# Kernel optimization log

Measured on AMD Instinct MI355X. Metric: run time of the kernel, lower is better.

The kernel has to match this reference:

```python
import jax, jax.numpy as jnp
import numpy as np

D_MODEL = 1024
N_HEAD = 16
ATT_DIM = D_MODEL // N_HEAD  # 64
B, S = 8, 2048


def setup_inputs() -> dict:
    key = jax.random.key(0)
    kq, kk, kv, kwq, kwk, kwv = jax.random.split(key, 6)
    # xavier_uniform bound for Linear(hidden_dim -> att_dim)
    bound = float(np.sqrt(6.0 / (D_MODEL + ATT_DIM)))
    return {
        "q": jax.random.normal(kq, (B, S, D_MODEL), dtype=jnp.float32),
        "k": jax.random.normal(kk, (B, S, D_MODEL), dtype=jnp.float32),
        "v": jax.random.normal(kv, (B, S, D_MODEL), dtype=jnp.float32),
        "Wq": jax.random.uniform(kwq, (ATT_DIM, D_MODEL), jnp.float32, -bound, bound),
        "Wk": jax.random.uniform(kwk, (ATT_DIM, D_MODEL), jnp.float32, -bound, bound),
        "Wv": jax.random.uniform(kwv, (ATT_DIM, D_MODEL), jnp.float32, -bound, bound),
    }


def reference(q, k, v, Wq, Wk, Wv):
    # Linear projections (no bias): [B,S,d_model] @ [d_model,att_dim]
    qp = jnp.einsum('bsd,ed->bse', q, Wq)
    kp = jnp.einsum('bsd,ed->bse', k, Wk)
    vp = jnp.einsum('bsd,ed->bse', v, Wv)
    # Scores: note original divides by att_dim (not sqrt)
    scores = jnp.einsum('bqe,bke->bqk', qp, kp) / ATT_DIM
    probs = jax.nn.softmax(scores, axis=-1)  # [B,S,S]
    att = jnp.einsum('bqk,bke->bqe', probs, vp)  # [B,S,att_dim]
    # dropout is identity in eval mode
    return (att, probs)
```

## Files before the change

### kernel.cpp

```cpp
#include <hip/hip_runtime.h>
#include <hip/hip_bf16.h>

#define D_MODEL 1024
#define ATT_DIM 64
#define BATCH 8
#define SEQ 2048
#define MROWS (BATCH * SEQ)

typedef short bf16x8 __attribute__((ext_vector_type(8)));
typedef float f32x4 __attribute__((ext_vector_type(4)));

#define MFMA16(a, b, c) __builtin_amdgcn_mfma_f32_16x16x32_bf16((a), (b), (c), 0, 0, 0)

__device__ inline short f2bf(float f) {
    union { __hip_bfloat16 h; short s; } u;
    u.h = __float2bfloat16(f);
    return u.s;
}

__device__ __forceinline__ unsigned cvtpk(float lo, float hi) {
    unsigned r;
    asm("v_cvt_pk_bf16_f32 %0, %1, %2" : "=v"(r) : "v"(lo), "v"(hi));
    return r;
}

__device__ __forceinline__ void gload_lds16(const void* g, void* l) {
    __builtin_amdgcn_global_load_lds(
        (const __attribute__((address_space(1))) void*)g,
        (__attribute__((address_space(3))) void*)l, 16, 0, 0);
}

__global__ __launch_bounds__(256) void wcvt_kernel(
    const float* __restrict__ Wq, const float* __restrict__ Wk,
    const float* __restrict__ Wv, short* __restrict__ Wbf)
{
    const int idx = blockIdx.x * 256 + threadIdx.x;
    const int per = ATT_DIM * D_MODEL;
    const int base = idx * 8;
    const int mi = base / per;
    const int off = base - mi * per;
    const float* src = (mi == 0) ? Wq : (mi == 1 ? Wk : Wv);
    const float sc = (mi == 0) ? (1.0f / 64.0f) : 1.0f;
    const float4 a = *reinterpret_cast<const float4*>(src + off);
    const float4 b = *reinterpret_cast<const float4*>(src + off + 4);
    bf16x8 r;
    r[0] = f2bf(a.x * sc); r[1] = f2bf(a.y * sc);
    r[2] = f2bf(a.z * sc); r[3] = f2bf(a.w * sc);
    r[4] = f2bf(b.x * sc); r[5] = f2bf(b.y * sc);
    r[6] = f2bf(b.z * sc); r[7] = f2bf(b.w * sc);
    *reinterpret_cast<bf16x8*>(Wbf + base) = r;
}

__global__ __launch_bounds__(256) void proj_mfma_kernel(
    const float* __restrict__ q, const float* __restrict__ k,
    const float* __restrict__ v, const short* __restrict__ Wbf,
    short* __restrict__ qp, short* __restrict__ kp, short* __restrict__ vpT)
{
    const int mat = blockIdx.y;
    const float* x = (mat == 0) ? q : (mat == 1 ? k : v);
    const short* W = Wbf + mat * ATT_DIM * D_MODEL;

    __shared__ float As[2][4096];

    const int tid = threadIdx.x;
    const int w = tid >> 6;
    const int l = tid & 63;
    const int lr = l & 15;
    const int g = l >> 4;

    const int m0 = blockIdx.x * 64;
    const int row = w * 16 + lr;
    const int xr = (row & 7) << 4;

    f32x4 acc[4] = {};

    #define STAGE(c, buf)                                                      \
        {                                                                      \
            const int kt_ = (c) * 64;                                          \
            _Pragma("unroll")                                                  \
            for (int j = 0; j < 4; ++j) {                                      \
                const int rs = (w * 4 + j) * 4 + g;                            \
                const int scb = (lr * 16) ^ ((rs & 7) << 4);                   \
                gload_lds16(x + (long)(m0 + rs) * D_MODEL + kt_ + (scb >> 2),  \
                            &As[buf][(w * 4 + j) * 256]);                      \
            }                                                                  \
        }

    STAGE(0, 0);
    __syncthreads();

    for (int c = 0; c < 16; ++c) {
        const int buf = c & 1;
        if (c < 15) STAGE(c + 1, buf ^ 1);

        const int kt = c * 64;
        const char* Ab = (const char*)&As[buf][0] + row * 256;
        #pragma unroll
        for (int ks = 0; ks < 2; ++ks) {
            const int b0 = ks * 128 + g * 32;
            const float4 a0 = *reinterpret_cast<const float4*>(Ab + (b0 ^ xr));
            const float4 a1 = *reinterpret_cast<const float4*>(Ab + ((b0 + 16) ^ xr));
            bf16x8 af;
            af[0] = f2bf(a0.x); af[1] = f2bf(a0.y); af[2] = f2bf(a0.z); af[3] = f2bf(a0.w);
            af[4] = f2bf(a1.x); af[5] = f2bf(a1.y); af[6] = f2bf(a1.z); af[7] = f2bf(a1.w);
            #pragma unroll
            for (int ef = 0; ef < 4; ++ef) {
                const bf16x8 wf = *reinterpret_cast<const bf16x8*>(
                    W + (ef * 16 + lr) * D_MODEL + kt + ks * 32 + g * 8);
                acc[ef] = MFMA16(af, wf, acc[ef]);
            }
        }
        __syncthreads();
    }
    #undef STAGE

    if (mat < 2) {
        short* out = (mat == 0) ? qp : kp;
        #pragma unroll
        for (int ef = 0; ef < 4; ++ef)
            #pragma unroll
            for (int j = 0; j < 4; ++j)
                out[(long)(m0 + w * 16 + g * 4 + j) * ATT_DIM + ef * 16 + lr] =
                    f2bf(acc[ef][j]);
    } else {
        const int b = m0 / SEQ;
        const int s0 = (m0 - b * SEQ) + w * 16;
        #pragma unroll
        for (int ef = 0; ef < 4; ++ef)
            #pragma unroll
            for (int j = 0; j < 4; ++j)
                vpT[((long)b * ATT_DIM + ef * 16 + lr) * SEQ + s0 + g * 4 + j] =
                    f2bf(acc[ef][j]);
    }
}

__global__ __launch_bounds__(512, 4) void attn_kernel(
    const short* __restrict__ qp, const short* __restrict__ kp,
    const short* __restrict__ vpT, float* __restrict__ probs,
    float* __restrict__ att)
{
    __shared__ float stats_l[8][16];
    __shared__ float lds_o[8][64][17];

    const int tid = threadIdx.x;
    const int w = tid >> 6;
    const int l = tid & 63;
    const int lr = l & 15;
    const int g = l >> 4;

    const int b = blockIdx.y;
    const int q0 = blockIdx.x * 16;

    const short* qpb = qp + ((long)b * SEQ + q0) * ATT_DIM;
    const short* kpb = kp + (long)b * SEQ * ATT_DIM;
    const short* vTb = vpT + (long)b * ATT_DIM * SEQ;

    const bf16x8 qa0 = *reinterpret_cast<const bf16x8*>(qpb + lr * ATT_DIM + g * 8);
    const bf16x8 qa1 = *reinterpret_cast<const bf16x8*>(qpb + lr * ATT_DIM + 32 + g * 8);

    const int kbeg = w * 256;

    f32x4 s[8][2];
    #pragma unroll
    for (int ch = 0; ch < 8; ++ch) {
        const short* kb = kpb + (long)(kbeg + ch * 32) * ATT_DIM;
        const bf16x8 kb00 = *reinterpret_cast<const bf16x8*>(kb + lr * ATT_DIM + g * 8);
        const bf16x8 kb01 = *reinterpret_cast<const bf16x8*>(kb + lr * ATT_DIM + 32 + g * 8);
        const bf16x8 kb10 = *reinterpret_cast<const bf16x8*>(kb + (16 + lr) * ATT_DIM + g * 8);
        const bf16x8 kb11 = *reinterpret_cast<const bf16x8*>(kb + (16 + lr) * ATT_DIM + 32 + g * 8);
        f32x4 t0 = {}; t0 = MFMA16(kb00, qa0, t0); t0 = MFMA16(kb01, qa1, t0);
        f32x4 t1 = {}; t1 = MFMA16(kb10, qa0, t1); t1 = MFMA16(kb11, qa1, t1);
        s[ch][0] = t0; s[ch][1] = t1;
    }

    float lw = 0.f;
    #pragma unroll
    for (int ch = 0; ch < 8; ++ch)
        #pragma unroll
        for (int h = 0; h < 2; ++h)
            #pragma unroll
            for (int j = 0; j < 4; ++j) {
                const float e = __expf(s[ch][h][j]);
                s[ch][h][j] = e;
                lw += e;
            }
    lw += __shfl_xor(lw, 16);
    lw += __shfl_xor(lw, 32);

    if (l < 16) stats_l[w][l] = lw;
    __syncthreads();

    float tot = 0.f;
    #pragma unroll
    for (int ww = 0; ww < 8; ++ww) tot += stats_l[ww][lr];
    const float inv = 1.0f / tot;
    #pragma unroll
    for (int ch = 0; ch < 8; ++ch)
        #pragma unroll
        for (int h = 0; h < 2; ++h)
            s[ch][h] *= inv;

    f32x4 accO[4] = {};
    float* pbase = probs + ((long)b * SEQ + q0 + lr) * SEQ;
    const bool hi2 = (g & 2) != 0;
    const bool swp = ((g ^ (g >> 1)) & 1) != 0;
    const bool odd = (g & 1) != 0;

    #pragma unroll
    for (int ch = 0; ch < 8; ++ch) {
        const int k0 = kbeg + ch * 32;
        *reinterpret_cast<f32x4*>(pbase + k0 + g * 4)      = s[ch][0];
        *reinterpret_cast<f32x4*>(pbase + k0 + 16 + g * 4) = s[ch][1];

        const unsigned xy0 = cvtpk(s[ch][0][0], s[ch][0][1]);
        const unsigned xy1 = cvtpk(s[ch][0][2], s[ch][0][3]);
        const unsigned zw0 = cvtpk(s[ch][1][0], s[ch][1][1]);
        const unsigned zw1 = cvtpk(s[ch][1][2], s[ch][1][3]);

        const unsigned s1a = hi2 ? xy0 : zw0;
        const unsigned s1b = hi2 ? xy1 : zw1;
        const unsigned r1a = __shfl_xor(s1a, 32);
        const unsigned r1b = __shfl_xor(s1b, 32);
        const unsigned p1a = hi2 ? zw0 : xy0;
        const unsigned p1b = hi2 ? zw1 : xy1;
        const unsigned s2a = swp ? p1a : r1a;
        const unsigned s2b = swp ? p1b : r1b;
        const unsigned r2a = __shfl_xor(s2a, 16);
        const unsigned r2b = __shfl_xor(s2b, 16);
        const unsigned ka = swp ? r1a : p1a;
        const unsigned kb_ = swp ? r1b : p1b;
        const unsigned d0 = odd ? r2a : ka;
        const unsigned d1 = odd ? r2b : kb_;
        const unsigned d2 = odd ? ka : r2a;
        const unsigned d3 = odd ? kb_ : r2b;
        union { uint4 u4; bf16x8 v; } pbu;
        pbu.u4 = make_uint4(d0, d1, d2, d3);
        const bf16x8 pb = pbu.v;

        #pragma unroll
        for (int ef = 0; ef < 4; ++ef) {
            const bf16x8 va = *reinterpret_cast<const bf16x8*>(
                vTb + (long)(ef * 16 + lr) * SEQ + k0 + g * 8);
            accO[ef] = MFMA16(va, pb, accO[ef]);
        }
    }

    #pragma unroll
    for (int ef = 0; ef < 4; ++ef)
        #pragma unroll
        for (int j = 0; j < 4; ++j)
            lds_o[w][ef * 16 + g * 4 + j][lr] = accO[ef][j];
    __syncthreads();

    {
        const int qr = tid >> 5;
        const int e0 = (tid & 31) * 2;
        float o0 = 0.f, o1 = 0.f;
        #pragma unroll
        for (int ww = 0; ww < 8; ++ww) {
            o0 += lds_o[ww][e0][qr];
            o1 += lds_o[ww][e0 + 1][qr];
        }
        float2 o = make_float2(o0, o1);
        *reinterpret_cast<float2*>(att + ((long)b * SEQ + q0 + qr) * ATT_DIM + e0) = o;
    }
}

extern "C" void kernel_launch(void* const* d_in, const int* in_sizes, int n_in,
                              void* d_out, int out_size, void* d_ws, size_t ws_size,
                              hipStream_t stream)
{
    const float* q  = (const float*)d_in[0];
    const float* k  = (const float*)d_in[1];
    const float* v  = (const float*)d_in[2];
    const float* Wq = (const float*)d_in[3];
    const float* Wk = (const float*)d_in[4];
    const float* Wv = (const float*)d_in[5];

    float* att   = (float*)d_out;
    float* probs = att + (size_t)BATCH * SEQ * ATT_DIM;

    short* qp  = (short*)d_ws;
    short* kp  = qp + (size_t)MROWS * ATT_DIM;
    short* vpT = kp + (size_t)MROWS * ATT_DIM;
    short* Wbf = vpT + (size_t)MROWS * ATT_DIM;

    wcvt_kernel<<<dim3(96), 256, 0, stream>>>(Wq, Wk, Wv, Wbf);

    proj_mfma_kernel<<<dim3(MROWS / 64, 3), 256, 0, stream>>>(
        q, k, v, Wbf, qp, kp, vpT);

    attn_kernel<<<dim3(SEQ / 16, BATCH), 512, 0, stream>>>(
        qp, kp, vpT, probs, att);
}
```

Baseline: 145.9 us.

## Split projection K dimension across waves with LDS reduction, 16-row blocks

The projection kernel now gives each block 16 rows and has each of its four waves cover a quarter of the 1024-wide reduction dimension. All input is loaded into LDS up front, with no double-buffered loop. Partial sums are reduced through shared memory by wave 0, and the grid grows fourfold. The aim is more blocks and parallelism for this memory-bound projection, at the cost of no load/compute overlap within a block, an extra LDS reduction, and 80KB of LDS per block, which limits occupancy.

```diff
diff --git a/kernel.cpp b/kernel.cpp
--- a/kernel.cpp
+++ b/kernel.cpp
@@ -60,7 +60,8 @@
     const float* x = (mat == 0) ? q : (mat == 1 ? k : v);
     const short* W = Wbf + mat * ATT_DIM * D_MODEL;
 
-    __shared__ float As[2][4096];
+    __shared__ float As[4][16][256];
+    __shared__ float red[3][16][64];
 
     const int tid = threadIdx.x;
     const int w = tid >> 6;
@@ -68,51 +69,53 @@
     const int lr = l & 15;
     const int g = l >> 4;
 
-    const int m0 = blockIdx.x * 64;
-    const int row = w * 16 + lr;
-    const int xr = (row & 7) << 4;
+    const int m0 = blockIdx.x * 16;
+
+    #pragma unroll
+    for (int r = 0; r < 16; ++r) {
+        const int cb = (l * 16) ^ ((r & 7) << 4);
+        gload_lds16(x + (long)(m0 + r) * D_MODEL + w * 256 + (cb >> 2),
+                    &As[w][r][0]);
+    }
+    asm volatile("s_waitcnt vmcnt(0)" ::: "memory");
+    __builtin_amdgcn_sched_barrier(0);
 
     f32x4 acc[4] = {};
-
-    #define STAGE(c, buf)                                                      \
-        {                                                                      \
-            const int kt_ = (c) * 64;                                          \
-            _Pragma("unroll")                                                  \
-            for (int j = 0; j < 4; ++j) {                                      \
-                const int rs = (w * 4 + j) * 4 + g;                            \
-                const int scb = (lr * 16) ^ ((rs & 7) << 4);                   \
-                gload_lds16(x + (long)(m0 + rs) * D_MODEL + kt_ + (scb >> 2),  \
-                            &As[buf][(w * 4 + j) * 256]);                      \
-            }                                                                  \
+    const int xr = (lr & 7) << 4;
+    const char* Ab = (const char*)&As[w][lr][0];
+    #pragma unroll
+    for (int ks = 0; ks < 8; ++ks) {
+        const int b0 = ks * 128 + g * 32;
+        const float4 a0 = *reinterpret_cast<const float4*>(Ab + (b0 ^ xr));
+        const float4 a1 = *reinterpret_cast<const float4*>(Ab + ((b0 + 16) ^ xr));
+        bf16x8 af;
+        af[0] = f2bf(a0.x); af[1] = f2bf(a0.y); af[2] = f2bf(a0.z); af[3] = f2bf(a0.w);
+        af[4] = f2bf(a1.x); af[5] = f2bf(a1.y); af[6] = f2bf(a1.z); af[7] = f2bf(a1.w);
+        #pragma unroll
+        for (int ef = 0; ef < 4; ++ef) {
+            const bf16x8 wf = *reinterpret_cast<const bf16x8*>(
+                W + (ef * 16 + lr) * D_MODEL + w * 256 + ks * 32 + g * 8);
+            acc[ef] = MFMA16(af, wf, acc[ef]);
         }
-
-    STAGE(0, 0);
+    }
+
+    if (w > 0) {
+        #pragma unroll
+        for (int ef = 0; ef < 4; ++ef)
+            #pragma unroll
+            for (int j = 0; j < 4; ++j)
+                red[w - 1][g * 4 + j][ef * 16 + lr] = acc[ef][j];
+    }
     __syncthreads();
-
-    for (int c = 0; c < 16; ++c) {
-        const int buf = c & 1;
-        if (c < 15) STAGE(c + 1, buf ^ 1);
-
-        const int kt = c * 64;
-        const char* Ab = (const char*)&As[buf][0] + row * 256;
-        #pragma unroll
-        for (int ks = 0; ks < 2; ++ks) {
-            const int b0 = ks * 128 + g * 32;
-            const float4 a0 = *reinterpret_cast<const float4*>(Ab + (b0 ^ xr));
-            const float4 a1 = *reinterpret_cast<const float4*>(Ab + ((b0 + 16) ^ xr));
-            bf16x8 af;
-            af[0] = f2bf(a0.x); af[1] = f2bf(a0.y); af[2] = f2bf(a0.z); af[3] = f2bf(a0.w);
-            af[4] = f2bf(a1.x); af[5] = f2bf(a1.y); af[6] = f2bf(a1.z); af[7] = f2bf(a1.w);
-            #pragma unroll
-            for (int ef = 0; ef < 4; ++ef) {
-                const bf16x8 wf = *reinterpret_cast<const bf16x8*>(
-                    W + (ef * 16 + lr) * D_MODEL + kt + ks * 32 + g * 8);
-                acc[ef] = MFMA16(af, wf, acc[ef]);
-            }
-        }
-        __syncthreads();
-    }
-    #undef STAGE
+    if (w != 0) return;
+
+    #pragma unroll
+    for (int ef = 0; ef < 4; ++ef)
+        #pragma unroll
+        for (int j = 0; j < 4; ++j)
+            acc[ef][j] += red[0][g * 4 + j][ef * 16 + lr] +
+                          red[1][g * 4 + j][ef * 16 + lr] +
+                          red[2][g * 4 + j][ef * 16 + lr];
 
     if (mat < 2) {
         short* out = (mat == 0) ? qp : kp;
@@ -120,11 +123,11 @@
         for (int ef = 0; ef < 4; ++ef)
             #pragma unroll
             for (int j = 0; j < 4; ++j)
-                out[(long)(m0 + w * 16 + g * 4 + j) * ATT_DIM + ef * 16 + lr] =
+                out[(long)(m0 + g * 4 + j) * ATT_DIM + ef * 16 + lr] =
                     f2bf(acc[ef][j]);
     } else {
         const int b = m0 / SEQ;
-        const int s0 = (m0 - b * SEQ) + w * 16;
+        const int s0 = m0 - b * SEQ;
         #pragma unroll
         for (int ef = 0; ef < 4; ++ef)
             #pragma unroll
@@ -287,7 +290,7 @@
 
     wcvt_kernel<<<dim3(96), 256, 0, stream>>>(Wq, Wk, Wv, Wbf);
 
-    proj_mfma_kernel<<<dim3(MROWS / 64, 3), 256, 0, stream>>>(
+    proj_mfma_kernel<<<dim3(MROWS / 16, 3), 256, 0, stream>>>(
         q, k, v, Wbf, qp, kp, vpT);
 
     attn_kernel<<<dim3(SEQ / 16, BATCH), 512, 0, stream>>>(
```

Measured after the change: 163.9 us. 12.4% more time.
